# Kernel tuning notes

Hardware: AMD Instinct MI355X
Metric: run time of the kernel (lower is better)

## Reference

```python
import jax, jax.numpy as jnp
import numpy as np

B, N, K, D, A, V = 2, 32768, 16, 256, 64, 64


def setup_inputs() -> dict:
    key = jax.random.key(0)
    ks = jax.random.split(key, 20)
    r = lambda i, shape: jax.random.normal(ks[i], shape, jnp.float32) * 0.02
    return dict(
        x=jax.random.normal(ks[0], (B, N, D), jnp.float32),
        knn_idx=jax.random.randint(ks[1], (N, K), 0, N),
        knn_rel_pos=jax.random.normal(ks[2], (N, K, 3), jnp.float32),
        g1=jnp.ones((D,), jnp.float32), b1=jnp.zeros((D,), jnp.float32),
        g2=jnp.ones((D,), jnp.float32), b2=jnp.zeros((D,), jnp.float32),
        Wq=r(3, (D, A)), bq=jnp.zeros((A,), jnp.float32),
        Wk=r(4, (D, A)), bk=jnp.zeros((A,), jnp.float32),
        Wv=r(5, (D, V)), bv=jnp.zeros((V,), jnp.float32),
        Wo=r(6, (V, D)), bo=jnp.zeros((D,), jnp.float32),
        Wpa1=r(7, (3, A)), bpa1=jnp.zeros((A,), jnp.float32),
        Wpa2=r(8, (A, A)), bpa2=jnp.zeros((A,), jnp.float32),
        Wpv1=r(9, (3, V)), bpv1=jnp.zeros((V,), jnp.float32),
        Wpv2=r(10, (V, V)), bpv2=jnp.zeros((V,), jnp.float32),
        Ws1=r(11, (A, A)), bs1=jnp.zeros((A,), jnp.float32),
        Ws2=r(12, (A, 1)), bs2=jnp.zeros((1,), jnp.float32),
        Wf1=r(13, (D, 2 * D)), bf1=jnpp if False else jnp.zeros((2 * D,), jnp.float32),
        Wf2=r(14, (2 * D, D)), bf2=jnp.zeros((D,), jnp.float32),
    )


def _ln(t, g, b):
    m = t.mean(-1, keepdims=True)
    var = ((t - m) ** 2).mean(-1, keepdims=True)
    return (t - m) * jax.lax.rsqrt(var + 1e-5) * g + b


def reference(x, knn_idx, knn_rel_pos, g1, b1, g2, b2,
              Wq, bq, Wk, bk, Wv, bv, Wo, bo,
              Wpa1, bpa1, Wpa2, bpa2, Wpv1, bpv1, Wpv2, bpv2,
              Ws1, bs1, Ws2, bs2, Wf1, bf1, Wf2, bf2):
    scale = jnp.sqrt(jnp.float32(A))
    h = _ln(x, g1, b1)                       # [B,N,D]
    q = h @ Wq + bq                          # [B,N,A]
    k_all = h @ Wk + bk                      # [B,N,A]
    v_all = h @ Wv + bv                      # [B,N,V]
    kn = k_all[:, knn_idx]                   # gather -> [B,N,K,A]
    vn = v_all[:, knn_idx]                   # [B,N,K,V]
    ra = jax.nn.relu(knn_rel_pos @ Wpa1 + bpa1) @ Wpa2 + bpa2  # [N,K,A]
    rv = jax.nn.relu(knn_rel_pos @ Wpv1 + bpv1) @ Wpv2 + bpv2  # [N,K,V]
    t = jnp.tanh(q[:, :, None, :] - kn + ra[None])             # [B,N,K,A]
    score = (jax.nn.relu(t @ Ws1 + bs1) @ Ws2 + bs2)[..., 0]   # [B,N,K]
    attn = jax.nn.softmax(score / scale, axis=2)
    ctx = jnp.einsum('bnk,bnkv->bnv', attn, vn + rv[None])     # [B,N,V]
    x = x + ctx @ Wo + bo
    h2 = _ln(x, g2, b2)
    x = x + (jax.nn.gelu(h2 @ Wf1 + bf1, approximate=False) @ Wf2 + bf2)
    return x
```

## Files before the change

kernel.cpp:

```cpp
#include <hip/hip_runtime.h>
#include <hip/hip_bf16.h>
#include <math.h>

#define BB 2
#define NN 32768
#define KK 16
#define DD 256
#define AA 64
#define VV 64

typedef __attribute__((ext_vector_type(8))) short bf16x8;
typedef __attribute__((ext_vector_type(4))) float f32x4;
typedef __attribute__((ext_vector_type(4))) unsigned short u16x4;

__device__ __forceinline__ ushort f2bf(float v) {
  __hip_bfloat16 b = __float2bfloat16(v);
  ushort u; __builtin_memcpy(&u, &b, 2);
  return u;
}
__device__ __forceinline__ float bflo(unsigned u) { return __uint_as_float(u << 16); }
__device__ __forceinline__ float bfhi(unsigned u) { return __uint_as_float(u & 0xffff0000u); }

__device__ __forceinline__ void astore2(ushort* A, int row, int colpair, float lo, float hi) {
  int off = (row * 128 + colpair * 4) ^ ((row & 7) << 4);
  unsigned u = ((unsigned)f2bf(hi) << 16) | (unsigned)f2bf(lo);
  *reinterpret_cast<unsigned*>(reinterpret_cast<char*>(A) + off) = u;
}
__device__ __forceinline__ void zstore8(ushort* A, int row, int chunk) {
  int off = (row * 128 + chunk * 8) ^ ((row & 7) << 4);
  *reinterpret_cast<unsigned long long*>(reinterpret_cast<char*>(A) + off) = 0ULL;
}
__device__ __forceinline__ bf16x8 afrag(const ushort* A, int rowbase, int lane, int ks) {
  int row = rowbase + (lane & 15), g = lane >> 4;
  int off = (row * 128 + ks * 64 + g * 16) ^ ((row & 7) << 4);
  return *reinterpret_cast<const bf16x8*>(reinterpret_cast<const char*>(A) + off);
}
__device__ __forceinline__ bf16x8 loadfrag(const ushort* p, int fi, int lane) {
  return *reinterpret_cast<const bf16x8*>(&p[((size_t)fi * 64 + lane) * 8]);
}

__global__ __launch_bounds__(256) void k_prep(
    const float* __restrict__ Wq, const float* __restrict__ Wk, const float* __restrict__ Wv,
    const float* __restrict__ Wf1, const float* __restrict__ Wf2,
    const float* __restrict__ Wpa2, const float* __restrict__ Wpv2,
    const float* __restrict__ Ws1, const float* __restrict__ Wo,
    ushort* __restrict__ pQKV, ushort* __restrict__ pWf1, ushort* __restrict__ pWf2,
    ushort* __restrict__ pS, ushort* __restrict__ pWo) {
  int tid = blockIdx.x * 256 + threadIdx.x;
  int lane = tid & 63, g = lane >> 4, c16 = lane & 15;
  bf16x8 f;
  if (tid < 6144) {
    int fi = tid >> 6; int ks = fi / 12, nt = fi % 12;
    int col = nt * 16 + c16;
    const float* W = (col < 64) ? Wq : (col < 128) ? Wk : Wv;
    int c = col & 63;
#pragma unroll
    for (int e = 0; e < 8; e++) f[e] = (short)f2bf(W[(ks * 32 + g * 8 + e) * 64 + c]);
    *reinterpret_cast<bf16x8*>(&pQKV[(size_t)tid * 8]) = f;
  } else if (tid < 22528) {
    int t2 = tid - 6144; int fi = t2 >> 6; int ks = fi >> 5, nt = fi & 31;
    int col = nt * 16 + c16;
#pragma unroll
    for (int e = 0; e < 8; e++) f[e] = (short)f2bf(Wf1[(ks * 32 + g * 8 + e) * 512 + col]);
    *reinterpret_cast<bf16x8*>(&pWf1[(size_t)t2 * 8]) = f;
  } else if (tid < 38912) {
    int t3 = tid - 22528; int fi = t3 >> 6; int ks = fi >> 4, nt = fi & 15;
    int col = nt * 16 + c16;
#pragma unroll
    for (int e = 0; e < 8; e++) f[e] = (short)f2bf(Wf2[(ks * 32 + g * 8 + e) * 256 + col]);
    *reinterpret_cast<bf16x8*>(&pWf2[(size_t)t3 * 8]) = f;
  } else if (tid < 40448) {
    int t4 = tid - 38912; int fi = t4 >> 6;
    int mat = fi >> 3, ks = (fi >> 2) & 1, nt = fi & 3;
    const float* W = (mat == 0) ? Wpa2 : (mat == 1) ? Wpv2 : Ws1;
    int col = nt * 16 + c16;
#pragma unroll
    for (int e = 0; e < 8; e++) f[e] = (short)f2bf(W[(ks * 32 + g * 8 + e) * 64 + col]);
    *reinterpret_cast<bf16x8*>(&pS[(size_t)t4 * 8]) = f;
  } else if (tid < 42496) {
    int t5 = tid - 40448; int fi = t5 >> 6; int ks = fi >> 4, nt = fi & 15;
    int col = nt * 16 + c16;
#pragma unroll
    for (int e = 0; e < 8; e++) f[e] = (short)f2bf(Wo[(ks * 32 + g * 8 + e) * 256 + col]);
    *reinterpret_cast<bf16x8*>(&pWo[(size_t)t5 * 8]) = f;
  }
}

__global__ __launch_bounds__(256) void k_qkv(
    const float* __restrict__ x, const float* __restrict__ g1, const float* __restrict__ b1,
    const ushort* __restrict__ pW,
    const float* __restrict__ bq, const float* __restrict__ bk, const float* __restrict__ bv,
    ushort* __restrict__ qo, ushort* __restrict__ ko, ushort* __restrict__ vo) {
  __shared__ __align__(16) ushort hs[32 * 256];
  int t = threadIdx.x, lane = t & 63, w = t >> 6;
  size_t row0 = (size_t)blockIdx.x * 32;

  {
    const float4 gv = *reinterpret_cast<const float4*>(&g1[lane * 4]);
    const float4 bvv = *reinterpret_cast<const float4*>(&b1[lane * 4]);
#pragma unroll
    for (int r8 = 0; r8 < 8; r8++) {
      int r = w * 8 + r8;
      const float4 xv = *reinterpret_cast<const float4*>(&x[(row0 + r) * DD + lane * 4]);
      float s = xv.x + xv.y + xv.z + xv.w;
      float s2 = xv.x * xv.x + xv.y * xv.y + xv.z * xv.z + xv.w * xv.w;
      for (int o = 32; o > 0; o >>= 1) { s += __shfl_down(s, o, 64); s2 += __shfl_down(s2, o, 64); }
      s = __shfl(s, 0, 64); s2 = __shfl(s2, 0, 64);
      float m = s * (1.f / DD), rs = rsqrtf(s2 * (1.f / DD) - m * m + 1e-5f);
      u16x4 hv;
      hv[0] = f2bf((xv.x - m) * rs * gv.x + bvv.x);
      hv[1] = f2bf((xv.y - m) * rs * gv.y + bvv.y);
      hv[2] = f2bf((xv.z - m) * rs * gv.z + bvv.z);
      hv[3] = f2bf((xv.w - m) * rs * gv.w + bvv.w);
      int off = (r * 512 + lane * 8) ^ ((r & 7) << 4);
      *reinterpret_cast<u16x4*>(reinterpret_cast<char*>(hs) + off) = hv;
    }
  }
  __syncthreads();

  f32x4 acc[2][3] = {};
  bf16x8 fw[3][3];
  int rowa = lane & 15, gg = lane >> 4;
#pragma unroll
  for (int p = 0; p < 2; p++)
#pragma unroll
    for (int j = 0; j < 3; j++) fw[p][j] = loadfrag(pW, p * 12 + w * 3 + j, lane);
#pragma unroll
  for (int ks = 0; ks < 8; ks++) {
    if (ks + 2 < 8) {
#pragma unroll
      for (int j = 0; j < 3; j++) fw[(ks + 2) % 3][j] = loadfrag(pW, (ks + 2) * 12 + w * 3 + j, lane);
    }
    bf16x8 a0 = *reinterpret_cast<const bf16x8*>(reinterpret_cast<const char*>(hs) +
                 ((rowa * 512 + ks * 64 + gg * 16) ^ ((rowa & 7) << 4)));
    bf16x8 a1 = *reinterpret_cast<const bf16x8*>(reinterpret_cast<const char*>(hs) +
                 (((rowa + 16) * 512 + ks * 64 + gg * 16) ^ ((rowa & 7) << 4)));
#pragma unroll
    for (int j = 0; j < 3; j++) {
      acc[0][j] = __builtin_amdgcn_mfma_f32_16x16x32_bf16(a0, fw[ks % 3][j], acc[0][j], 0, 0, 0);
      acc[1][j] = __builtin_amdgcn_mfma_f32_16x16x32_bf16(a1, fw[ks % 3][j], acc[1][j], 0, 0, 0);
    }
  }

#pragma unroll
  for (int j = 0; j < 3; j++) {
    int ntg = w * 3 + j;
    int buf = ntg >> 2;
    ushort* out = (buf == 0) ? qo : (buf == 1) ? ko : vo;
    const float* bias = (buf == 0) ? bq : (buf == 1) ? bk : bv;
    int col = (ntg & 3) * 16 + (lane & 15);
    float bb = bias[col];
#pragma unroll
    for (int mt = 0; mt < 2; mt++)
#pragma unroll
      for (int r = 0; r < 4; r++) {
        int row = mt * 16 + (lane >> 4) * 4 + r;
        out[(row0 + row) * 64 + col] = f2bf(acc[mt][j][r] + bb);
      }
  }
}

__global__ __launch_bounds__(256) void k_attn(
    const float* __restrict__ x, const float* __restrict__ relpos, const int* __restrict__ knn,
    const ushort* __restrict__ qg, const ushort* __restrict__ kg, const ushort* __restrict__ vg,
    const float* __restrict__ Wpa1, const float* __restrict__ bpa1, const float* __restrict__ bpa2,
    const float* __restrict__ Wpv1, const float* __restrict__ bpv1, const float* __restrict__ bpv2,
    const ushort* __restrict__ pS, const float* __restrict__ bs1,
    const float* __restrict__ Ws2, const float* __restrict__ bs2,
    const ushort* __restrict__ pWo, const float* __restrict__ bo,
    float* __restrict__ xmid) {
  int n0 = blockIdx.x * 2;
  int t = threadIdx.x, lane = t & 63, w = t >> 6;
  int g = lane >> 4, c16 = lane & 15;
  int c2 = lane & 31, kh = lane >> 5;

  __shared__ __align__(16) ushort A0[64 * 64];
  __shared__ __align__(16) ushort ra_bs[32][72];
  __shared__ __align__(16) ushort rv_bs[32][72];
  __shared__ float hidp[64][68];
  __shared__ __align__(16) ushort ctile[16 * 64];
  __shared__ __align__(8) float qv[4][64];
  __shared__ float attn_s[64];
  __shared__ float rp_s[2][48];
  __shared__ int idx_s[2][16];

  if (t < 32) idx_s[t >> 4][t & 15] = knn[(n0 + (t >> 4)) * KK + (t & 15)];
  if (t >= 64 && t < 160) {
    int i = t - 64;
    rp_s[i / 48][i % 48] = relpos[(size_t)n0 * 48 + i];
  }
  if (t >= 160 && t < 160 + 192) {
    int i = t - 160;
    zstore8(ctile, 4 + (i >> 4), i & 15);
  }
  qv[w][lane] = bflo(qg[((size_t)(w & 1) * NN + n0 + (w >> 1)) * AA + lane]);
  __syncthreads();

  {
    const float* W1 = (w < 2) ? Wpa1 : Wpv1;
    const float* bb1 = (w < 2) ? bpa1 : bpv1;
    int pt = w & 1;
    int base = (w < 2 ? 0 : 32) + pt * 16;
    float2 w0 = *reinterpret_cast<const float2*>(&W1[2 * c2]);
    float2 w1 = *reinterpret_cast<const float2*>(&W1[64 + 2 * c2]);
    float2 w2 = *reinterpret_cast<const float2*>(&W1[128 + 2 * c2]);
    float2 bb = *reinterpret_cast<const float2*>(&bb1[2 * c2]);
#pragma unroll
    for (int j = 0; j < 8; j++) {
      int k = kh * 8 + j;
      float r0 = rp_s[pt][k * 3], r1 = rp_s[pt][k * 3 + 1], r2 = rp_s[pt][k * 3 + 2];
      float lo = fmaxf(bb.x + r0 * w0.x + r1 * w1.x + r2 * w2.x, 0.f);
      float hi = fmaxf(bb.y + r0 * w0.y + r1 * w1.y + r2 * w2.y, 0.f);
      astore2(A0, base + k, c2, lo, hi);
    }
  }
  __syncthreads();

  {
    bf16x8 bwa0 = loadfrag(pS, 0 + w, lane);
    bf16x8 bwa1 = loadfrag(pS, 4 + w, lane);
    bf16x8 bwv0 = loadfrag(pS, 8 + w, lane);
    bf16x8 bwv1 = loadfrag(pS, 12 + w, lane);
    int col = w * 16 + c16;
    float ba2 = bpa2[col], bv2 = bpv2[col];
#pragma unroll
    for (int mt = 0; mt < 2; mt++) {
      bf16x8 a0 = afrag(A0, mt * 16, lane, 0), a1 = afrag(A0, mt * 16, lane, 1);
      f32x4 acc = {0.f, 0.f, 0.f, 0.f};
      acc = __builtin_amdgcn_mfma_f32_16x16x32_bf16(a0, bwa0, acc, 0, 0, 0);
      acc = __builtin_amdgcn_mfma_f32_16x16x32_bf16(a1, bwa1, acc, 0, 0, 0);
#pragma unroll
      for (int r = 0; r < 4; r++) ra_bs[mt * 16 + g * 4 + r][col] = f2bf(acc[r] + ba2);
      bf16x8 v0 = afrag(A0, 32 + mt * 16, lane, 0), v1 = afrag(A0, 32 + mt * 16, lane, 1);
      f32x4 accv = {0.f, 0.f, 0.f, 0.f};
      accv = __builtin_amdgcn_mfma_f32_16x16x32_bf16(v0, bwv0, accv, 0, 0, 0);
      accv = __builtin_amdgcn_mfma_f32_16x16x32_bf16(v1, bwv1, accv, 0, 0, 0);
#pragma unroll
      for (int r = 0; r < 4; r++) rv_bs[mt * 16 + g * 4 + r][col] = f2bf(accv[r] + bv2);
    }
  }
  __syncthreads();

  {
    int pt = w >> 1, b = w & 1;
    float2 qq = *reinterpret_cast<const float2*>(&qv[w][2 * c2]);
    size_t bbase = (size_t)b * NN;
#pragma unroll
    for (int j = 0; j < 8; j++) {
      int k = kh * 8 + j;
      const ushort* krow = kg + (bbase + idx_s[pt][k]) * AA;
      unsigned ku = *reinterpret_cast<const unsigned*>(&krow[2 * c2]);
      unsigned ru = *reinterpret_cast<const unsigned*>(&ra_bs[pt * 16 + k][2 * c2]);
      float x0 = qq.x - bflo(ku) + bflo(ru);
      float x1 = qq.y - bfhi(ku) + bfhi(ru);
      float t0 = 1.f - 2.f * __builtin_amdgcn_rcpf(__expf(2.f * x0) + 1.f);
      float t1 = 1.f - 2.f * __builtin_amdgcn_rcpf(__expf(2.f * x1) + 1.f);
      astore2(A0, w * 16 + k, c2, t0, t1);
    }
  }
  __syncthreads();

  {
    bf16x8 fsA = loadfrag(pS, 16 + w, lane);
    bf16x8 fsB = loadfrag(pS, 20 + w, lane);
    int col = w * 16 + c16;
    float bsc = bs1[col], wsc = Ws2[col];
#pragma unroll
    for (int mt = 0; mt < 4; mt++) {
      bf16x8 a0 = afrag(A0, mt * 16, lane, 0), a1 = afrag(A0, mt * 16, lane, 1);
      f32x4 acc = {0.f, 0.f, 0.f, 0.f};
      acc = __builtin_amdgcn_mfma_f32_16x16x32_bf16(a0, fsA, acc, 0, 0, 0);
      acc = __builtin_amdgcn_mfma_f32_16x16x32_bf16(a1, fsB, acc, 0, 0, 0);
#pragma unroll
      for (int r = 0; r < 4; r++)
        hidp[mt * 16 + g * 4 + r][col] = fmaxf(acc[r] + bsc, 0.f) * wsc;
    }
  }
  __syncthreads();

  if (t < 64) {
    float s = 0.f;
#pragma unroll
    for (int c = 0; c < 16; c++) {
      float4 v4 = *reinterpret_cast<const float4*>(&hidp[t][c * 4]);
      s += v4.x + v4.y + v4.z + v4.w;
    }
    float sc = (s + bs2[0]) * 0.125f;
    float mx = sc;
#pragma unroll
    for (int o = 8; o > 0; o >>= 1) mx = fmaxf(mx, __shfl_xor(mx, o, 64));
    float e = __expf(sc - mx);
    float ss = e;
#pragma unroll
    for (int o = 8; o > 0; o >>= 1) ss += __shfl_xor(ss, o, 64);
    attn_s[t] = e / ss;
  }
  __syncthreads();

  {
    int pt = w >> 1, b = w & 1;
    size_t bbase = (size_t)b * NN;
    float a0 = 0.f, a1 = 0.f;
#pragma unroll
    for (int j = 0; j < 8; j++) {
      int k = kh * 8 + j;
      const ushort* vrow = vg + (bbase + idx_s[pt][k]) * VV;
      unsigned vu = *reinterpret_cast<const unsigned*>(&vrow[2 * c2]);
      unsigned ru = *reinterpret_cast<const unsigned*>(&rv_bs[pt * 16 + k][2 * c2]);
      float aw = attn_s[w * 16 + k];
      a0 += aw * (bflo(vu) + bflo(ru));
      a1 += aw * (bfhi(vu) + bfhi(ru));
    }
    a0 += __shfl_xor(a0, 32, 64);
    a1 += __shfl_xor(a1, 32, 64);
    if (kh == 0) astore2(ctile, w, c2, a0, a1);
  }
  __syncthreads();

  {
    bf16x8 a0 = afrag(ctile, 0, lane, 0), a1 = afrag(ctile, 0, lane, 1);
    f32x4 acc[4];
#pragma unroll
    for (int j = 0; j < 4; j++) {
      bf16x8 b0 = loadfrag(pWo, 0 + w * 4 + j, lane);
      bf16x8 b1 = loadfrag(pWo, 16 + w * 4 + j, lane);
      f32x4 a = {0.f, 0.f, 0.f, 0.f};
      a = __builtin_amdgcn_mfma_f32_16x16x32_bf16(a0, b0, a, 0, 0, 0);
      a = __builtin_amdgcn_mfma_f32_16x16x32_bf16(a1, b1, a, 0, 0, 0);
      acc[j] = a;
    }
    if (g == 0) {
#pragma unroll
      for (int j = 0; j < 4; j++) {
        int col = w * 64 + j * 16 + c16;
        float bb = bo[col];
#pragma unroll
        for (int r = 0; r < 4; r++) {
          int pt = r >> 1, b = r & 1;
          size_t addr = ((size_t)b * NN + n0 + pt) * DD + col;
          xmid[addr] = x[addr] + acc[j][r] + bb;
        }
      }
    }
  }
}

__global__ __launch_bounds__(256) void k_ffn(
    const float* __restrict__ xmid, const float* __restrict__ g2, const float* __restrict__ b2,
    const ushort* __restrict__ pWf1, const float* __restrict__ bf1,
    const ushort* __restrict__ pWf2, const float* __restrict__ bf2,
    float* __restrict__ out) {
  __shared__ __align__(16) ushort hs[32 * 256];
  __shared__ __align__(16) ushort ys[32 * 512];
  int t = threadIdx.x, lane = t & 63, w = t >> 6;
  size_t row0 = (size_t)blockIdx.x * 32;
  int rowa = lane & 15, gg = lane >> 4;

  {
    const float4 gv = *reinterpret_cast<const float4*>(&g2[lane * 4]);
    const float4 bvv = *reinterpret_cast<const float4*>(&b2[lane * 4]);
#pragma unroll
    for (int r8 = 0; r8 < 8; r8++) {
      int r = w * 8 + r8;
      const float4 xv = *reinterpret_cast<const float4*>(&xmid[(row0 + r) * DD + lane * 4]);
      float s = xv.x + xv.y + xv.z + xv.w;
      float s2 = xv.x * xv.x + xv.y * xv.y + xv.z * xv.z + xv.w * xv.w;
      for (int o = 32; o > 0; o >>= 1) { s += __shfl_down(s, o, 64); s2 += __shfl_down(s2, o, 64); }
      s = __shfl(s, 0, 64); s2 = __shfl(s2, 0, 64);
      float m = s * (1.f / DD), rs = rsqrtf(s2 * (1.f / DD) - m * m + 1e-5f);
      u16x4 hv;
      hv[0] = f2bf((xv.x - m) * rs * gv.x + bvv.x);
      hv[1] = f2bf((xv.y - m) * rs * gv.y + bvv.y);
      hv[2] = f2bf((xv.z - m) * rs * gv.z + bvv.z);
      hv[3] = f2bf((xv.w - m) * rs * gv.w + bvv.w);
      int off = (r * 512 + lane * 8) ^ ((r & 7) << 4);
      *reinterpret_cast<u16x4*>(reinterpret_cast<char*>(hs) + off) = hv;
    }
  }
  __syncthreads();

  f32x4 acc1[2][8] = {};
  {
    bf16x8 fA[8], fB[8];
#pragma unroll
    for (int j = 0; j < 8; j++) fA[j] = loadfrag(pWf1, w * 8 + j, lane);
#pragma unroll
    for (int ks = 0; ks < 8; ks += 2) {
#pragma unroll
      for (int j = 0; j < 8; j++) fB[j] = loadfrag(pWf1, (ks + 1) * 32 + w * 8 + j, lane);
      {
        bf16x8 a0 = *reinterpret_cast<const bf16x8*>(reinterpret_cast<const char*>(hs) +
                     ((rowa * 512 + ks * 64 + gg * 16) ^ ((rowa & 7) << 4)));
        bf16x8 a1 = *reinterpret_cast<const bf16x8*>(reinterpret_cast<const char*>(hs) +
                     (((rowa + 16) * 512 + ks * 64 + gg * 16) ^ ((rowa & 7) << 4)));
#pragma unroll
        for (int j = 0; j < 8; j++) {
          acc1[0][j] = __builtin_amdgcn_mfma_f32_16x16x32_bf16(a0, fA[j], acc1[0][j], 0, 0, 0);
          acc1[1][j] = __builtin_amdgcn_mfma_f32_16x16x32_bf16(a1, fA[j], acc1[1][j], 0, 0, 0);
        }
      }
      if (ks + 2 < 8) {
#pragma unroll
        for (int j = 0; j < 8; j++) fA[j] = loadfrag(pWf1, (ks + 2) * 32 + w * 8 + j, lane);
      }
      {
        bf16x8 a0 = *reinterpret_cast<const bf16x8*>(reinterpret_cast<const char*>(hs) +
                     ((rowa * 512 + (ks + 1) * 64 + gg * 16) ^ ((rowa & 7) << 4)));
        bf16x8 a1 = *reinterpret_cast<const bf16x8*>(reinterpret_cast<const char*>(hs) +
                     (((rowa + 16) * 512 + (ks + 1) * 64 + gg * 16) ^ ((rowa & 7) << 4)));
#pragma unroll
        for (int j = 0; j < 8; j++) {
          acc1[0][j] = __builtin_amdgcn_mfma_f32_16x16x32_bf16(a0, fB[j], acc1[0][j], 0, 0, 0);
          acc1[1][j] = __builtin_amdgcn_mfma_f32_16x16x32_bf16(a1, fB[j], acc1[1][j], 0, 0, 0);
        }
      }
    }
  }

#pragma unroll
  for (int j = 0; j < 8; j++) {
    int col = w * 128 + j * 16 + (lane & 15);
    float bb = bf1[col];
#pragma unroll
    for (int mt = 0; mt < 2; mt++)
#pragma unroll
      for (int r = 0; r < 4; r++) {
        float v = acc1[mt][j][r] + bb;
        v = v * 0.5f * (1.f + erff(v * 0.70710678118654752f));
        int row = mt * 16 + (lane >> 4) * 4 + r;
        int off = (row * 1024 + col * 2) ^ ((row & 7) << 4);
        *reinterpret_cast<ushort*>(reinterpret_cast<char*>(ys) + off) = f2bf(v);
      }
  }
  __syncthreads();

  f32x4 acc2[2][4] = {};
  {
    bf16x8 f2[3][4];
#pragma unroll
    for (int p = 0; p < 2; p++)
#pragma unroll
      for (int j = 0; j < 4; j++) f2[p][j] = loadfrag(pWf2, p * 16 + w * 4 + j, lane);
#pragma unroll
    for (int ks = 0; ks < 16; ks++) {
      if (ks + 2 < 16) {
#pragma unroll
        for (int j = 0; j < 4; j++) f2[(ks + 2) % 3][j] = loadfrag(pWf2, (ks + 2) * 16 + w * 4 + j, lane);
      }
      bf16x8 a0 = *reinterpret_cast<const bf16x8*>(reinterpret_cast<const char*>(ys) +
                   ((rowa * 1024 + ks * 64 + gg * 16) ^ ((rowa & 7) << 4)));
      bf16x8 a1 = *reinterpret_cast<const bf16x8*>(reinterpret_cast<const char*>(ys) +
                   (((rowa + 16) * 1024 + ks * 64 + gg * 16) ^ ((rowa & 7) << 4)));
#pragma unroll
      for (int j = 0; j < 4; j++) {
        acc2[0][j] = __builtin_amdgcn_mfma_f32_16x16x32_bf16(a0, f2[ks % 3][j], acc2[0][j], 0, 0, 0);
        acc2[1][j] = __builtin_amdgcn_mfma_f32_16x16x32_bf16(a1, f2[ks % 3][j], acc2[1][j], 0, 0, 0);
      }
    }
  }

#pragma unroll
  for (int j = 0; j < 4; j++) {
    int col = w * 64 + j * 16 + (lane & 15);
    float bb = bf2[col];
#pragma unroll
    for (int mt = 0; mt < 2; mt++)
#pragma unroll
      for (int r = 0; r < 4; r++) {
        int row = mt * 16 + (lane >> 4) * 4 + r;
        size_t idx = (row0 + row) * DD + col;
        out[idx] = xmid[idx] + acc2[mt][j][r] + bb;
      }
  }
}

extern "C" void kernel_launch(void* const* d_in, const int* in_sizes, int n_in,
                              void* d_out, int out_size, void* d_ws, size_t ws_size,
                              hipStream_t stream) {
  const float* x      = (const float*)d_in[0];
  const int*   knn    = (const int*)  d_in[1];
  const float* relpos = (const float*)d_in[2];
  const float* g1     = (const float*)d_in[3];
  const float* b1     = (const float*)d_in[4];
  const float* g2     = (const float*)d_in[5];
  const float* b2     = (const float*)d_in[6];
  const float* Wq     = (const float*)d_in[7];
  const float* bq     = (const float*)d_in[8];
  const float* Wk     = (const float*)d_in[9];
  const float* bk     = (const float*)d_in[10];
  const float* Wv     = (const float*)d_in[11];
  const float* bv     = (const float*)d_in[12];
  const float* Wo     = (const float*)d_in[13];
  const float* bo     = (const float*)d_in[14];
  const float* Wpa1   = (const float*)d_in[15];
  const float* bpa1   = (const float*)d_in[16];
  const float* Wpa2   = (const float*)d_in[17];
  const float* bpa2   = (const float*)d_in[18];
  const float* Wpv1   = (const float*)d_in[19];
  const float* bpv1   = (const float*)d_in[20];
  const float* Wpv2   = (const float*)d_in[21];
  const float* bpv2   = (const float*)d_in[22];
  const float* Ws1    = (const float*)d_in[23];
  const float* bs1    = (const float*)d_in[24];
  const float* Ws2    = (const float*)d_in[25];
  const float* bs2    = (const float*)d_in[26];
  const float* Wf1    = (const float*)d_in[27];
  const float* bf1    = (const float*)d_in[28];
  const float* Wf2    = (const float*)d_in[29];
  const float* bf2    = (const float*)d_in[30];

  ushort* qb = (ushort*)d_ws;
  ushort* kb = qb + (size_t)BB * NN * AA;
  ushort* vb = kb + (size_t)BB * NN * AA;
  float* xmid = (float*)(vb + (size_t)BB * NN * VV);
  ushort* pQKV = (ushort*)(xmid + (size_t)BB * NN * DD);
  ushort* pWf1 = pQKV + 49152;
  ushort* pWf2 = pWf1 + 131072;
  ushort* pS   = pWf2 + 131072;
  ushort* pWo  = pS + 12288;

  k_prep<<<166, 256, 0, stream>>>(Wq, Wk, Wv, Wf1, Wf2, Wpa2, Wpv2, Ws1, Wo,
                                  pQKV, pWf1, pWf2, pS, pWo);
  k_qkv<<<(BB * NN) / 32, 256, 0, stream>>>(x, g1, b1, pQKV, bq, bk, bv, qb, kb, vb);
  k_attn<<<NN / 2, 256, 0, stream>>>(x, relpos, knn, qb, kb, vb,
                                     Wpa1, bpa1, bpa2, Wpv1, bpv1, bpv2,
                                     pS, bs1, Ws2, bs2, pWo, bo, xmid);
  k_ffn<<<(BB * NN) / 32, 256, 0, stream>>>(xmid, g2, b2, pWf1, bf1, pWf2, bf2, (float*)d_out);
}
```

Before: 423.3 us.

## Compute position-MLP first layer with MFMA and prefetch gathered keys early

The first layer of the relative-position MLPs (3→64) now runs as a zero-padded bf16 MFMA on a packed relpos tile instead of scalar FMAs, with the weights prepacked in the prep kernel. The neighbor key gathers are issued into registers before the next barrier so their latency overlaps the position-MLP MFMAs. The score hidden buffer is also stored as bf16 instead of fp32, shrinking LDS use. Costs: extra registers for the prefetched keys, bf16 rounding of relpos and of the score partials, and the ctile zero-init was removed, which may matter if that tile is read uninitialized.

```diff
diff --git a/kernel.cpp b/kernel.cpp
--- a/kernel.cpp
+++ b/kernel.cpp
@@ -21,14 +21,14 @@
 __device__ __forceinline__ float bflo(unsigned u) { return __uint_as_float(u << 16); }
 __device__ __forceinline__ float bfhi(unsigned u) { return __uint_as_float(u & 0xffff0000u); }
 
+__device__ __forceinline__ void astore(ushort* A, int row, int col, float v) {
+  int off = (row * 128 + col * 2) ^ ((row & 7) << 4);
+  *reinterpret_cast<ushort*>(reinterpret_cast<char*>(A) + off) = f2bf(v);
+}
 __device__ __forceinline__ void astore2(ushort* A, int row, int colpair, float lo, float hi) {
   int off = (row * 128 + colpair * 4) ^ ((row & 7) << 4);
   unsigned u = ((unsigned)f2bf(hi) << 16) | (unsigned)f2bf(lo);
   *reinterpret_cast<unsigned*>(reinterpret_cast<char*>(A) + off) = u;
-}
-__device__ __forceinline__ void zstore8(ushort* A, int row, int chunk) {
-  int off = (row * 128 + chunk * 8) ^ ((row & 7) << 4);
-  *reinterpret_cast<unsigned long long*>(reinterpret_cast<char*>(A) + off) = 0ULL;
 }
 __device__ __forceinline__ bf16x8 afrag(const ushort* A, int rowbase, int lane, int ks) {
   int row = rowbase + (lane & 15), g = lane >> 4;
@@ -44,6 +44,7 @@
     const float* __restrict__ Wf1, const float* __restrict__ Wf2,
     const float* __restrict__ Wpa2, const float* __restrict__ Wpv2,
     const float* __restrict__ Ws1, const float* __restrict__ Wo,
+    const float* __restrict__ Wpa1, const float* __restrict__ Wpv1,
     ushort* __restrict__ pQKV, ushort* __restrict__ pWf1, ushort* __restrict__ pWf2,
     ushort* __restrict__ pS, ushort* __restrict__ pWo) {
   int tid = blockIdx.x * 256 + threadIdx.x;
@@ -69,16 +70,27 @@
 #pragma unroll
     for (int e = 0; e < 8; e++) f[e] = (short)f2bf(Wf2[(ks * 32 + g * 8 + e) * 256 + col]);
     *reinterpret_cast<bf16x8*>(&pWf2[(size_t)t3 * 8]) = f;
-  } else if (tid < 40448) {
+  } else if (tid < 40960) {
     int t4 = tid - 38912; int fi = t4 >> 6;
-    int mat = fi >> 3, ks = (fi >> 2) & 1, nt = fi & 3;
-    const float* W = (mat == 0) ? Wpa2 : (mat == 1) ? Wpv2 : Ws1;
-    int col = nt * 16 + c16;
-#pragma unroll
-    for (int e = 0; e < 8; e++) f[e] = (short)f2bf(W[(ks * 32 + g * 8 + e) * 64 + col]);
+    if (fi < 24) {
+      int mat = fi >> 3, ks = (fi >> 2) & 1, nt = fi & 3;
+      const float* W = (mat == 0) ? Wpa2 : (mat == 1) ? Wpv2 : Ws1;
+      int col = nt * 16 + c16;
+#pragma unroll
+      for (int e = 0; e < 8; e++) f[e] = (short)f2bf(W[(ks * 32 + g * 8 + e) * 64 + col]);
+    } else {
+      int mat = (fi - 24) >> 2, nt = fi & 3;
+      const float* W = mat ? Wpv1 : Wpa1;
+      int col = nt * 16 + c16;
+#pragma unroll
+      for (int e = 0; e < 8; e++) {
+        int K = g * 8 + e;
+        f[e] = (K < 3) ? (short)f2bf(W[K * 64 + col]) : (short)0;
+      }
+    }
     *reinterpret_cast<bf16x8*>(&pS[(size_t)t4 * 8]) = f;
-  } else if (tid < 42496) {
-    int t5 = tid - 40448; int fi = t5 >> 6; int ks = fi >> 4, nt = fi & 15;
+  } else if (tid < 43008) {
+    int t5 = tid - 40960; int fi = t5 >> 6; int ks = fi >> 4, nt = fi & 15;
     int col = nt * 16 + c16;
 #pragma unroll
     for (int e = 0; e < 8; e++) f[e] = (short)f2bf(Wo[(ks * 32 + g * 8 + e) * 256 + col]);
@@ -163,8 +175,8 @@
 __global__ __launch_bounds__(256) void k_attn(
     const float* __restrict__ x, const float* __restrict__ relpos, const int* __restrict__ knn,
     const ushort* __restrict__ qg, const ushort* __restrict__ kg, const ushort* __restrict__ vg,
-    const float* __restrict__ Wpa1, const float* __restrict__ bpa1, const float* __restrict__ bpa2,
-    const float* __restrict__ Wpv1, const float* __restrict__ bpv1, const float* __restrict__ bpv2,
+    const float* __restrict__ bpa1, const float* __restrict__ bpa2,
+    const float* __restrict__ bpv1, const float* __restrict__ bpv2,
     const ushort* __restrict__ pS, const float* __restrict__ bs1,
     const float* __restrict__ Ws2, const float* __restrict__ bs2,
     const ushort* __restrict__ pWo, const float* __restrict__ bo,
@@ -177,41 +189,60 @@
   __shared__ __align__(16) ushort A0[64 * 64];
   __shared__ __align__(16) ushort ra_bs[32][72];
   __shared__ __align__(16) ushort rv_bs[32][72];
-  __shared__ float hidp[64][68];
+  __shared__ __align__(16) ushort hid_bs[64][72];
+  __shared__ __align__(16) ushort RP[32 * 32];
   __shared__ __align__(16) ushort ctile[16 * 64];
   __shared__ __align__(8) float qv[4][64];
   __shared__ float attn_s[64];
-  __shared__ float rp_s[2][48];
   __shared__ int idx_s[2][16];
 
-  if (t < 32) idx_s[t >> 4][t & 15] = knn[(n0 + (t >> 4)) * KK + (t & 15)];
-  if (t >= 64 && t < 160) {
-    int i = t - 64;
-    rp_s[i / 48][i % 48] = relpos[(size_t)n0 * 48 + i];
-  }
-  if (t >= 160 && t < 160 + 192) {
-    int i = t - 160;
-    zstore8(ctile, 4 + (i >> 4), i & 15);
+  if (t < 32) {
+    idx_s[t >> 4][t & 15] = knn[(n0 + (t >> 4)) * KK + (t & 15)];
+    float r0 = relpos[(size_t)n0 * 48 + t * 3 + 0];
+    float r1 = relpos[(size_t)n0 * 48 + t * 3 + 1];
+    float r2 = relpos[(size_t)n0 * 48 + t * 3 + 2];
+    uint4 z; z.x = 0; z.y = 0; z.z = 0; z.w = 0;
+    uint4 f0;
+    f0.x = ((unsigned)f2bf(r1) << 16) | (unsigned)f2bf(r0);
+    f0.y = (unsigned)f2bf(r2);
+    f0.z = 0; f0.w = 0;
+    *reinterpret_cast<uint4*>(&RP[t * 32 + 0])  = f0;
+    *reinterpret_cast<uint4*>(&RP[t * 32 + 8])  = z;
+    *reinterpret_cast<uint4*>(&RP[t * 32 + 16]) = z;
+    *reinterpret_cast<uint4*>(&RP[t * 32 + 24]) = z;
   }
   qv[w][lane] = bflo(qg[((size_t)(w & 1) * NN + n0 + (w >> 1)) * AA + lane]);
   __syncthreads();
 
   {
-    const float* W1 = (w < 2) ? Wpa1 : Wpv1;
-    const float* bb1 = (w < 2) ? bpa1 : bpv1;
-    int pt = w & 1;
-    int base = (w < 2 ? 0 : 32) + pt * 16;
-    float2 w0 = *reinterpret_cast<const float2*>(&W1[2 * c2]);
-    float2 w1 = *reinterpret_cast<const float2*>(&W1[64 + 2 * c2]);
-    float2 w2 = *reinterpret_cast<const float2*>(&W1[128 + 2 * c2]);
-    float2 bb = *reinterpret_cast<const float2*>(&bb1[2 * c2]);
+    bf16x8 aRP0 = *reinterpret_cast<const bf16x8*>(&RP[(lane & 15) * 32 + g * 8]);
+    bf16x8 aRP1 = *reinterpret_cast<const bf16x8*>(&RP[((lane & 15) + 16) * 32 + g * 8]);
+    bf16x8 bA = loadfrag(pS, 24 + w, lane);
+    bf16x8 bV = loadfrag(pS, 28 + w, lane);
+    int col = w * 16 + c16;
+    float ba = bpa1[col], bv1_ = bpv1[col];
+    f32x4 zz = {0.f, 0.f, 0.f, 0.f};
+    f32x4 hA0 = __builtin_amdgcn_mfma_f32_16x16x32_bf16(aRP0, bA, zz, 0, 0, 0);
+    f32x4 hA1 = __builtin_amdgcn_mfma_f32_16x16x32_bf16(aRP1, bA, zz, 0, 0, 0);
+    f32x4 hV0 = __builtin_amdgcn_mfma_f32_16x16x32_bf16(aRP0, bV, zz, 0, 0, 0);
+    f32x4 hV1 = __builtin_amdgcn_mfma_f32_16x16x32_bf16(aRP1, bV, zz, 0, 0, 0);
+#pragma unroll
+    for (int r = 0; r < 4; r++) {
+      astore(A0, 0  + g * 4 + r, col, fmaxf(hA0[r] + ba, 0.f));
+      astore(A0, 16 + g * 4 + r, col, fmaxf(hA1[r] + ba, 0.f));
+      astore(A0, 32 + g * 4 + r, col, fmaxf(hV0[r] + bv1_, 0.f));
+      astore(A0, 48 + g * 4 + r, col, fmaxf(hV1[r] + bv1_, 0.f));
+    }
+  }
+
+  unsigned kuval[8];
+  {
+    int pt3 = w >> 1, b3 = w & 1;
+    size_t bbase = (size_t)b3 * NN;
 #pragma unroll
     for (int j = 0; j < 8; j++) {
       int k = kh * 8 + j;
-      float r0 = rp_s[pt][k * 3], r1 = rp_s[pt][k * 3 + 1], r2 = rp_s[pt][k * 3 + 2];
-      float lo = fmaxf(bb.x + r0 * w0.x + r1 * w1.x + r2 * w2.x, 0.f);
-      float hi = fmaxf(bb.y + r0 * w0.y + r1 * w1.y + r2 * w2.y, 0.f);
-      astore2(A0, base + k, c2, lo, hi);
+      kuval[j] = *reinterpret_cast<const unsigned*>(&kg[(bbase + idx_s[pt3][k]) * AA + 2 * c2]);
     }
   }
   __syncthreads();
@@ -242,14 +273,12 @@
   __syncthreads();
 
   {
-    int pt = w >> 1, b = w & 1;
+    int pt = w >> 1;
     float2 qq = *reinterpret_cast<const float2*>(&qv[w][2 * c2]);
-    size_t bbase = (size_t)b * NN;
 #pragma unroll
     for (int j = 0; j < 8; j++) {
       int k = kh * 8 + j;
-      const ushort* krow = kg + (bbase + idx_s[pt][k]) * AA;
-      unsigned ku = *reinterpret_cast<const unsigned*>(&krow[2 * c2]);
+      unsigned ku = kuval[j];
       unsigned ru = *reinterpret_cast<const unsigned*>(&ra_bs[pt * 16 + k][2 * c2]);
       float x0 = qq.x - bflo(ku) + bflo(ru);
       float x1 = qq.y - bfhi(ku) + bfhi(ru);
@@ -273,17 +302,19 @@
       acc = __builtin_amdgcn_mfma_f32_16x16x32_bf16(a1, fsB, acc, 0, 0, 0);
 #pragma unroll
       for (int r = 0; r < 4; r++)
-        hidp[mt * 16 + g * 4 + r][col] = fmaxf(acc[r] + bsc, 0.f) * wsc;
+        hid_bs[mt * 16 + g * 4 + r][col] = f2bf(fmaxf(acc[r] + bsc, 0.f) * wsc);
     }
   }
   __syncthreads();
 
   if (t < 64) {
+    const uint4* hrow = reinterpret_cast<const uint4*>(&hid_bs[t][0]);
     float s = 0.f;
 #pragma unroll
-    for (int c = 0; c < 16; c++) {
-      float4 v4 = *reinterpret_cast<const float4*>(&hidp[t][c * 4]);
-      s += v4.x + v4.y + v4.z + v4.w;
+    for (int c = 0; c < 8; c++) {
+      uint4 v4 = hrow[c];
+      s += bflo(v4.x) + bfhi(v4.x) + bflo(v4.y) + bfhi(v4.y) +
+           bflo(v4.z) + bfhi(v4.z) + bflo(v4.w) + bfhi(v4.w);
     }
     float sc = (s + bs2[0]) * 0.125f;
     float mx = sc;
@@ -517,13 +548,13 @@
   ushort* pWf1 = pQKV + 49152;
   ushort* pWf2 = pWf1 + 131072;
   ushort* pS   = pWf2 + 131072;
-  ushort* pWo  = pS + 12288;
-
-  k_prep<<<166, 256, 0, stream>>>(Wq, Wk, Wv, Wf1, Wf2, Wpa2, Wpv2, Ws1, Wo,
+  ushort* pWo  = pS + 16384;
+
+  k_prep<<<168, 256, 0, stream>>>(Wq, Wk, Wv, Wf1, Wf2, Wpa2, Wpv2, Ws1, Wo, Wpa1, Wpv1,
                                   pQKV, pWf1, pWf2, pS, pWo);
   k_qkv<<<(BB * NN) / 32, 256, 0, stream>>>(x, g1, b1, pQKV, bq, bk, bv, qb, kb, vb);
   k_attn<<<NN / 2, 256, 0, stream>>>(x, relpos, knn, qb, kb, vb,
-                                     Wpa1, bpa1, bpa2, Wpv1, bpv1, bpv2,
+                                     bpa1, bpa2, bpv1, bpv2,
                                      pS, bs1, Ws2, bs2, pWo, bo, xmid);
   k_ffn<<<(BB * NN) / 32, 256, 0, stream>>>(xmid, g2, b2, pWf1, bf1, pWf2, bf2, (float*)d_out);
 }
```

After: 420.1 us. No clear change (-0.8%).
